# Kernel tuning notes

Hardware: AMD Instinct MI355X
Metric: run time of the kernel (lower is better)

## Reference

```python
import jax, jax.numpy as jnp
import numpy as np

D = 128
K = 8
TEMPERATURE = 1.0
LN_EPS = 1e-5
NORM_EPS = 1e-12


def setup_inputs() -> dict:
    key = jax.random.key(0)
    ks = jax.random.split(key, 6)
    B = 262144
    global_prosody = jax.random.normal(ks[0], (B, D), dtype=jnp.float32)
    W = jax.random.normal(ks[1], (D, D), dtype=jnp.float32) / np.sqrt(D)
    b = jnp.zeros((D,), dtype=jnp.float32)
    gamma = jnp.ones((D,), dtype=jnp.float32)
    beta = jnp.zeros((D,), dtype=jnp.float32)
    # codebook initialized as rows of an orthonormal basis (SVD of random init)
    init = jax.random.normal(ks[2], (D, K), dtype=jnp.float32)
    U, _, _ = jnp.linalg.svd(init, full_matrices=False)
    codebook = U[:, :K].T  # (K, D)
    return {"global_prosody": global_prosody, "W": W, "b": b,
            "gamma": gamma, "beta": beta, "codebook": codebook}


def _l2norm(x, axis=-1):
    n = jnp.sqrt(jnp.sum(x * x, axis=axis, keepdims=True))
    return x / jnp.maximum(n, NORM_EPS)


def reference(global_prosody, W, b, gamma, beta, codebook):
    # proj: Linear + LayerNorm
    h = global_prosody @ W.T + b                      # (B, D)
    mu = jnp.mean(h, axis=-1, keepdims=True)
    var = jnp.var(h, axis=-1, keepdims=True)
    h = (h - mu) / jnp.sqrt(var + LN_EPS) * gamma + beta
    # cosine-sim logits
    h_norm = _l2norm(h)                               # (B, D)
    cb_norm = _l2norm(codebook)                       # (K, D)
    logits = (h_norm @ cb_norm.T) / TEMPERATURE       # (B, K)
    soft_assign = jax.nn.softmax(logits, axis=-1)
    hard_indices = jnp.argmax(logits, axis=-1)        # (B,)
    hard_assign = jax.nn.one_hot(hard_indices, K, dtype=jnp.float32)
    # straight-through assignment
    assign = hard_assign + soft_assign - jax.lax.stop_gradient(soft_assign)
    embedding = assign @ codebook                     # (B, D)
    return hard_indices, soft_assign, embedding, logits
```

## Files before the change

### kernel.cpp

```cpp
#include <hip/hip_runtime.h>
#include <math.h>

#define DD 128
#define KK 8
#define LN_EPS 1e-5f
#define NORM_EPS 1e-12f

typedef __attribute__((ext_vector_type(8))) short bf16x8;
typedef __attribute__((ext_vector_type(4))) float f32x4;
typedef unsigned int uint;
typedef unsigned short ushort;

#define WSA_USHORTS (3 * 9 * 4 * 64 * 8)
#define G2B_OFF_F   (110592 / 4)
#define SCAL_OFF_F  (111616 / 4)

__device__ inline void split3(float x, uint& h, uint& m, uint& l) {
    uint u0 = __float_as_uint(x);
    uint rh = (u0 + 0x7FFFu + ((u0 >> 16) & 1u)) & 0xFFFF0000u;
    float xh = __uint_as_float(rh);
    float r1 = x - xh;
    uint u1 = __float_as_uint(r1);
    uint rm = (u1 + 0x7FFFu + ((u1 >> 16) & 1u)) & 0xFFFF0000u;
    float xm = __uint_as_float(rm);
    float r2 = r1 - xm;
    uint u2 = __float_as_uint(r2);
    uint rl = (u2 + 0x7FFFu + ((u2 >> 16) & 1u));
    h = rh; m = rm; l = rl;
}

__device__ inline void split2pack(float e0, float e1, uint& ph, uint& pm, uint& pl) {
    uint h0, m0, l0, h1, m1, l1;
    split3(e0, h0, m0, l0);
    split3(e1, h1, m1, l1);
    ph = (h0 >> 16) | (h1 & 0xFFFF0000u);
    pm = (m0 >> 16) | (m1 & 0xFFFF0000u);
    pl = (l0 >> 16) | (l1 & 0xFFFF0000u);
}

union FragU { uint4 u; bf16x8 f; };
union AccU  { f32x4 v; float a[4]; };

__global__ void l1q_prep0(const float* __restrict__ b, const float* __restrict__ gamma,
                          const float* __restrict__ beta, const float* __restrict__ cb,
                          float* __restrict__ ws)
{
    __shared__ float invn_s[KK];
    const int t = threadIdx.x;
    if (t < KK) {
        float s = 0.f;
        for (int j = 0; j < DD; ++j) { float v = cb[t * DD + j]; s = fmaf(v, v, s); }
        invn_s[t] = 1.0f / fmaxf(sqrtf(s), NORM_EPS);
    }
    __syncthreads();
    {
        float g = gamma[t];
        float* g2b = ws + G2B_OFF_F;
        g2b[2 * t]     = g * g;
        g2b[2 * t + 1] = b[t];
    }
    float* scal = ws + SCAL_OFF_F;
    if (t < KK) {
        float in = invn_s[t];
        float p = 0.f, q = 0.f, cu = 0.f;
        for (int j = 0; j < DD; ++j) {
            float c = cb[t * DD + j] * in;
            p  = fmaf(c, gamma[j], p);
            q  = fmaf(c, beta[j], q);
            cu = fmaf(c * gamma[j], b[j], cu);
        }
        scal[t]      = p;
        scal[8 + t]  = q;
        scal[22 + t] = cu;
    }
    if (t == 16) { float s = 0.f; for (int j = 0; j < DD; ++j) { float g = gamma[j]; s = fmaf(g, g, s); } scal[16] = s; }
    if (t == 17) { float s = 0.f; for (int j = 0; j < DD; ++j) s = fmaf(gamma[j], beta[j], s); scal[17] = s; }
    if (t == 18) { float s = 0.f; for (int j = 0; j < DD; ++j) { float v = beta[j]; s = fmaf(v, v, s); } scal[18] = s; }
    if (t == 19) { float s = 0.f; for (int j = 0; j < DD; ++j) s += b[j]; scal[19] = s; }
    if (t == 20) { float s = 0.f; for (int j = 0; j < DD; ++j) s = fmaf(gamma[j] * gamma[j], b[j], s); scal[20] = s; }
    if (t == 21) { float s = 0.f; for (int j = 0; j < DD; ++j) s = fmaf(gamma[j] * beta[j], b[j], s); scal[21] = s; }
}

__global__ void l1q_prepA(const float* __restrict__ W, const float* __restrict__ b,
                          const float* __restrict__ gamma, const float* __restrict__ beta,
                          const float* __restrict__ cb, ushort* __restrict__ wsA)
{
    __shared__ float invn_s[KK];
    __shared__ float we[11][DD];
    __shared__ float wext[16][32];
    const int t = threadIdx.x;
    const int jt = blockIdx.x >> 2;
    const int ks = blockIdx.x & 3;

    if (jt == 8) {
        if (t < KK) {
            float s = 0.f;
            for (int j = 0; j < DD; ++j) { float v = cb[t * DD + j]; s = fmaf(v, v, s); }
            invn_s[t] = 1.0f / fmaxf(sqrtf(s), NORM_EPS);
        }
        __syncthreads();
        for (int idx = t; idx < 11 * DD; idx += 256) {
            int e = idx / DD, j = idx % DD;
            float g = gamma[j];
            float v;
            if (e == 0)      v = 1.0f;
            else if (e == 1) v = g * g;
            else if (e == 2) v = g * beta[j];
            else             v = cb[(e - 3) * DD + j] * invn_s[e - 3] * g;
            we[e][j] = v;
        }
        __syncthreads();
    }

    for (int idx = t; idx < 512; idx += 256) {
        int jl = idx >> 5, kk = idx & 31;
        int k = ks * 32 + kk;
        float val;
        if (jt < 8) {
            val = W[(jt * 16 + jl) * DD + k];
        } else if (jl < 11) {
            float s = 0.f;
            for (int j = 0; j < DD; ++j) s = fmaf(we[jl][j], W[j * DD + k], s);
            val = s;
        } else {
            val = 0.f;
        }
        wext[jl][kk] = val;
    }
    __syncthreads();

    for (int idx = t; idx < 512; idx += 256) {
        int jl = idx >> 5, kk = idx & 31;
        int quad = kk >> 3, i = kk & 7;
        int lane = quad * 16 + jl;
        uint h, m, l;
        split3(wext[jl][kk], h, m, l);
        int base = jt * 4 + ks;
        wsA[(0 * 36 + base) * 512 + lane * 8 + i] = (ushort)(h >> 16);
        wsA[(1 * 36 + base) * 512 + lane * 8 + i] = (ushort)(m >> 16);
        wsA[(2 * 36 + base) * 512 + lane * 8 + i] = (ushort)(l >> 16);
    }
}

__global__ __launch_bounds__(256, 2)
void l1q_main(const float* __restrict__ x, const ushort* __restrict__ wsA,
              const float* __restrict__ wsf, const float* __restrict__ cb,
              float* __restrict__ out_idx, float* __restrict__ out_soft,
              float* __restrict__ out_emb, float* __restrict__ out_log,
              int B)
{
    __shared__ float g2b_s[256];
    __shared__ float scal_s[32];
    __shared__ float gath[4][320];
    __shared__ int   besti[4][64];

    const int t = threadIdx.x;
    const int wave = t >> 6;
    const int lane = t & 63;
    const int ml = lane & 15;
    const int q  = lane >> 4;
    const int rowbase = blockIdx.x * 256 + wave * 64;

    g2b_s[t] = wsf[G2B_OFF_F + t];
    if (t < 32) scal_s[t] = wsf[SCAL_OFF_F + t];
    __syncthreads();

    f32x4 acc[4][9];
    #pragma unroll
    for (int s = 0; s < 4; ++s)
        #pragma unroll
        for (int jt = 0; jt < 9; ++jt)
            acc[s][jt] = (f32x4){0.f, 0.f, 0.f, 0.f};

    for (int ks = 0; ks < 4; ++ks) {
        FragU xh[4], xm[4], xl[4];
        #pragma unroll
        for (int s = 0; s < 4; ++s) {
            const float* xp = x + (size_t)(rowbase + s * 16 + ml) * DD + ks * 32 + q * 8;
            float4 a = *(const float4*)xp;
            float4 c = *(const float4*)(xp + 4);
            split2pack(a.x, a.y, xh[s].u.x, xm[s].u.x, xl[s].u.x);
            split2pack(a.z, a.w, xh[s].u.y, xm[s].u.y, xl[s].u.y);
            split2pack(c.x, c.y, xh[s].u.z, xm[s].u.z, xl[s].u.z);
            split2pack(c.z, c.w, xh[s].u.w, xm[s].u.w, xl[s].u.w);
        }
        #pragma unroll
        for (int jt = 0; jt < 9; ++jt) {
            const int base = (jt * 4 + ks) * 512 + lane * 8;
            FragU wh, wm, wl;
            wh.u = *(const uint4*)(wsA + 0 * 36 * 512 + base);
            wm.u = *(const uint4*)(wsA + 1 * 36 * 512 + base);
            wl.u = *(const uint4*)(wsA + 2 * 36 * 512 + base);
            #pragma unroll
            for (int s = 0; s < 4; ++s) {
                f32x4 c = acc[s][jt];
                c = __builtin_amdgcn_mfma_f32_16x16x32_bf16(wl.f, xh[s].f, c, 0, 0, 0);
                c = __builtin_amdgcn_mfma_f32_16x16x32_bf16(wh.f, xl[s].f, c, 0, 0, 0);
                c = __builtin_amdgcn_mfma_f32_16x16x32_bf16(wm.f, xm[s].f, c, 0, 0, 0);
                c = __builtin_amdgcn_mfma_f32_16x16x32_bf16(wm.f, xh[s].f, c, 0, 0, 0);
                c = __builtin_amdgcn_mfma_f32_16x16x32_bf16(wh.f, xm[s].f, c, 0, 0, 0);
                c = __builtin_amdgcn_mfma_f32_16x16x32_bf16(wh.f, xh[s].f, c, 0, 0, 0);
                acc[s][jt] = c;
            }
        }
    }

    float s2a[4] = {0.f, 0.f, 0.f, 0.f};
    float t2a[4] = {0.f, 0.f, 0.f, 0.f};
    #pragma unroll
    for (int jt = 0; jt < 8; ++jt) {
        #pragma unroll
        for (int r = 0; r < 4; ++r) {
            int j = jt * 16 + q * 4 + r;
            float2 gb = *(const float2*)&g2b_s[2 * j];
            #pragma unroll
            for (int s = 0; s < 4; ++s) {
                AccU a; a.v = acc[s][jt];
                float h = a.a[r] + gb.y;
                float h2 = h * h;
                s2a[s] += h2;
                t2a[s] = fmaf(gb.x, h2, t2a[s]);
            }
        }
    }
    #pragma unroll
    for (int s = 0; s < 4; ++s) {
        s2a[s] += __shfl_xor(s2a[s], 16);
        s2a[s] += __shfl_xor(s2a[s], 32);
        t2a[s] += __shfl_xor(t2a[s], 16);
        t2a[s] += __shfl_xor(t2a[s], 32);
    }

    const float inv128 = 1.0f / 128.0f;
    const float cg2s = scal_s[16], cgbs = scal_s[17], cb2s = scal_s[18];
    const float cs1 = scal_s[19], ct1 = scal_s[20], cr1 = scal_s[21];

    #pragma unroll
    for (int s = 0; s < 4; ++s) {
        AccU mine; mine.v = acc[s][8];
        *(float4*)&gath[wave][ml * 20 + q * 4] = *(float4*)mine.a;
        __builtin_amdgcn_s_waitcnt(0);
        float4 A = *(const float4*)&gath[wave][ml * 20 + 0];
        float4 Bv = *(const float4*)&gath[wave][ml * 20 + 4];
        float4 C = *(const float4*)&gath[wave][ml * 20 + 8];

        float s1  = A.x + cs1;
        float t1  = A.y + ct1;
        float r1v = A.z + cr1;
        float u[KK] = {A.w + scal_s[22], Bv.x + scal_s[23], Bv.y + scal_s[24],
                       Bv.z + scal_s[25], Bv.w + scal_s[26], C.x + scal_s[27],
                       C.y + scal_s[28], C.z + scal_s[29]};

        float mu = s1 * inv128;
        float var = fmaf(-mu, mu, s2a[s] * inv128);
        float istd = 1.0f / sqrtf(var + LN_EPS);
        float nrm2 = istd * istd * (t2a[s] - 2.f * mu * t1 + mu * mu * cg2s)
                   + 2.f * istd * (r1v - mu * cgbs) + cb2s;
        float rinv = 1.0f / fmaxf(sqrtf(fmaxf(nrm2, 0.f)), NORM_EPS);

        float lg[KK];
        #pragma unroll
        for (int k = 0; k < KK; ++k)
            lg[k] = (istd * (u[k] - mu * scal_s[k]) + scal_s[8 + k]) * rinv;

        float mx = lg[0]; int bi = 0;
        #pragma unroll
        for (int k = 1; k < KK; ++k) if (lg[k] > mx) { mx = lg[k]; bi = k; }

        float ex[KK], se = 0.f;
        #pragma unroll
        for (int k = 0; k < KK; ++k) { ex[k] = expf(lg[k] - mx); se += ex[k]; }
        float rse = 1.0f / se;

        const int m = rowbase + s * 16 + ml;
        if (q == 0) {
            out_idx[m] = (float)bi;
            *(float4*)&out_log[(size_t)m * KK + 4] = make_float4(lg[4], lg[5], lg[6], lg[7]);
            besti[wave][s * 16 + ml] = bi;
        } else if (q == 1) {
            *(float4*)&out_soft[(size_t)m * KK] = make_float4(ex[0] * rse, ex[1] * rse, ex[2] * rse, ex[3] * rse);
        } else if (q == 2) {
            *(float4*)&out_soft[(size_t)m * KK + 4] = make_float4(ex[4] * rse, ex[5] * rse, ex[6] * rse, ex[7] * rse);
        } else {
            *(float4*)&out_log[(size_t)m * KK] = make_float4(lg[0], lg[1], lg[2], lg[3]);
        }
    }

    __builtin_amdgcn_s_waitcnt(0);
    const float4* cb4 = (const float4*)cb;
    float4* eo = (float4*)out_emb;
    #pragma unroll
    for (int s = 0; s < 4; ++s) {
        #pragma unroll
        for (int i = 0; i < 4; ++i) {
            int f4 = lane + 64 * i;
            int rl = f4 >> 5;
            int c  = f4 & 31;
            int k0 = besti[wave][s * 16 + rl];
            eo[(size_t)(rowbase + s * 16 + rl) * 32 + c] = cb4[k0 * 32 + c];
            int rl2 = (f4 + 256) >> 5;
            int k1 = besti[wave][s * 16 + rl2];
            eo[(size_t)(rowbase + s * 16 + rl2) * 32 + c] = cb4[k1 * 32 + c];
        }
    }
}

extern "C" void kernel_launch(void* const* d_in, const int* in_sizes, int n_in,
                              void* d_out, int out_size, void* d_ws, size_t ws_size,
                              hipStream_t stream) {
    const float* x     = (const float*)d_in[0];
    const float* W     = (const float*)d_in[1];
    const float* b     = (const float*)d_in[2];
    const float* gamma = (const float*)d_in[3];
    const float* beta  = (const float*)d_in[4];
    const float* cb    = (const float*)d_in[5];
    const int B = in_sizes[0] / DD;

    float*  ws  = (float*)d_ws;
    ushort* wsA = (ushort*)d_ws;

    float* out    = (float*)d_out;
    float* o_idx  = out;
    float* o_soft = out + (size_t)B;
    float* o_emb  = out + (size_t)B * (1 + KK);
    float* o_log  = out + (size_t)B * (1 + KK + DD);

    hipLaunchKernelGGL(l1q_prep0, dim3(1), dim3(128), 0, stream, b, gamma, beta, cb, ws);
    hipLaunchKernelGGL(l1q_prepA, dim3(36), dim3(256), 0, stream, W, b, gamma, beta, cb, wsA);
    const int grid = B / 256;
    hipLaunchKernelGGL(l1q_main, dim3(grid), dim3(256), 0, stream,
                       x, wsA, ws, cb, o_idx, o_soft, o_emb, o_log, B);
}
```

Before: 351.7 us.

## Stage split weights in LDS, use 16-row waves with 1024-thread blocks

The main kernel now runs 1024-thread blocks where each wave handles 16 rows instead of 64. The three-way bf16 split of W (about 108 KB) is copied into LDS once per block rather than read from global or L2 by every wave. The x row loads are software-prefetched one k-step ahead, and the x split switches to truncation plus v_perm packing instead of round-to-nearest bit arithmetic. This trades per-wave register reuse of W fragments across four row tiles for LDS reads and higher occupancy. It risks LDS capacity limits and a large staging cost per 256-row block.

```diff
diff --git a/kernel.cpp b/kernel.cpp
--- a/kernel.cpp
+++ b/kernel.cpp
@@ -11,7 +11,6 @@
 typedef unsigned int uint;
 typedef unsigned short ushort;
 
-#define WSA_USHORTS (3 * 9 * 4 * 64 * 8)
 #define G2B_OFF_F   (110592 / 4)
 #define SCAL_OFF_F  (111616 / 4)
 
@@ -29,13 +28,27 @@
     h = rh; m = rm; l = rl;
 }
 
-__device__ inline void split2pack(float e0, float e1, uint& ph, uint& pm, uint& pl) {
+__device__ inline void split3t(float x, uint& h, uint& m, uint& l) {
+    uint u0 = __float_as_uint(x);
+    float xh = __uint_as_float(u0 & 0xFFFF0000u);
+    float r1 = x - xh;
+    uint u1 = __float_as_uint(r1);
+    float xm = __uint_as_float(u1 & 0xFFFF0000u);
+    float r2 = r1 - xm;
+    h = u0; m = u1; l = __float_as_uint(r2);
+}
+
+__device__ inline uint packhi(uint a1, uint a0) {
+    return __builtin_amdgcn_perm(a1, a0, 0x07060302u);
+}
+
+__device__ inline void split2packt(float e0, float e1, uint& ph, uint& pm, uint& pl) {
     uint h0, m0, l0, h1, m1, l1;
-    split3(e0, h0, m0, l0);
-    split3(e1, h1, m1, l1);
-    ph = (h0 >> 16) | (h1 & 0xFFFF0000u);
-    pm = (m0 >> 16) | (m1 & 0xFFFF0000u);
-    pl = (l0 >> 16) | (l1 & 0xFFFF0000u);
+    split3t(e0, h0, m0, l0);
+    split3t(e1, h1, m1, l1);
+    ph = packhi(h1, h0);
+    pm = packhi(m1, m0);
+    pl = packhi(l1, l0);
 }
 
 union FragU { uint4 u; bf16x8 f; };
@@ -142,166 +155,158 @@
     }
 }
 
-__global__ __launch_bounds__(256, 2)
+__global__ __launch_bounds__(1024, 4)
 void l1q_main(const float* __restrict__ x, const ushort* __restrict__ wsA,
               const float* __restrict__ wsf, const float* __restrict__ cb,
               float* __restrict__ out_idx, float* __restrict__ out_soft,
               float* __restrict__ out_emb, float* __restrict__ out_log,
               int B)
 {
+    __shared__ uint4 Wl4[6912];
+    __shared__ float gath[16][320];
+    __shared__ int   besti[16][16];
     __shared__ float g2b_s[256];
     __shared__ float scal_s[32];
-    __shared__ float gath[4][320];
-    __shared__ int   besti[4][64];
 
     const int t = threadIdx.x;
     const int wave = t >> 6;
     const int lane = t & 63;
     const int ml = lane & 15;
     const int q  = lane >> 4;
-    const int rowbase = blockIdx.x * 256 + wave * 64;
-
-    g2b_s[t] = wsf[G2B_OFF_F + t];
-    if (t < 32) scal_s[t] = wsf[SCAL_OFF_F + t];
+    const int rowbase = blockIdx.x * 256 + wave * 16;
+    const int row = rowbase + ml;
+
+    const float* xp = x + (size_t)row * DD + q * 8;
+    float4 ra = *(const float4*)(xp + 0);
+    float4 rc = *(const float4*)(xp + 4);
+
+    {
+        const uint4* src = (const uint4*)wsA;
+        #pragma unroll
+        for (int i = 0; i < 7; ++i) {
+            int idx = t + i * 1024;
+            if (idx < 6912) Wl4[idx] = src[idx];
+        }
+    }
+    if (t < 256) g2b_s[t] = wsf[G2B_OFF_F + t];
+    if (t < 32)  scal_s[t] = wsf[SCAL_OFF_F + t];
     __syncthreads();
 
-    f32x4 acc[4][9];
-    #pragma unroll
-    for (int s = 0; s < 4; ++s)
-        #pragma unroll
-        for (int jt = 0; jt < 9; ++jt)
-            acc[s][jt] = (f32x4){0.f, 0.f, 0.f, 0.f};
-
+    f32x4 acc[9];
+    #pragma unroll
+    for (int jt = 0; jt < 9; ++jt) acc[jt] = (f32x4){0.f, 0.f, 0.f, 0.f};
+
+    #pragma unroll
     for (int ks = 0; ks < 4; ++ks) {
-        FragU xh[4], xm[4], xl[4];
-        #pragma unroll
-        for (int s = 0; s < 4; ++s) {
-            const float* xp = x + (size_t)(rowbase + s * 16 + ml) * DD + ks * 32 + q * 8;
-            float4 a = *(const float4*)xp;
-            float4 c = *(const float4*)(xp + 4);
-            split2pack(a.x, a.y, xh[s].u.x, xm[s].u.x, xl[s].u.x);
-            split2pack(a.z, a.w, xh[s].u.y, xm[s].u.y, xl[s].u.y);
-            split2pack(c.x, c.y, xh[s].u.z, xm[s].u.z, xl[s].u.z);
-            split2pack(c.z, c.w, xh[s].u.w, xm[s].u.w, xl[s].u.w);
-        }
+        int kn = ks < 3 ? ks + 1 : 3;
+        float4 na = *(const float4*)(xp + kn * 32 + 0);
+        float4 nc = *(const float4*)(xp + kn * 32 + 4);
+
+        FragU xh, xm, xl;
+        split2packt(ra.x, ra.y, xh.u.x, xm.u.x, xl.u.x);
+        split2packt(ra.z, ra.w, xh.u.y, xm.u.y, xl.u.y);
+        split2packt(rc.x, rc.y, xh.u.z, xm.u.z, xl.u.z);
+        split2packt(rc.z, rc.w, xh.u.w, xm.u.w, xl.u.w);
+
         #pragma unroll
         for (int jt = 0; jt < 9; ++jt) {
-            const int base = (jt * 4 + ks) * 512 + lane * 8;
+            const int pl = jt * 4 + ks;
             FragU wh, wm, wl;
-            wh.u = *(const uint4*)(wsA + 0 * 36 * 512 + base);
-            wm.u = *(const uint4*)(wsA + 1 * 36 * 512 + base);
-            wl.u = *(const uint4*)(wsA + 2 * 36 * 512 + base);
-            #pragma unroll
-            for (int s = 0; s < 4; ++s) {
-                f32x4 c = acc[s][jt];
-                c = __builtin_amdgcn_mfma_f32_16x16x32_bf16(wl.f, xh[s].f, c, 0, 0, 0);
-                c = __builtin_amdgcn_mfma_f32_16x16x32_bf16(wh.f, xl[s].f, c, 0, 0, 0);
-                c = __builtin_amdgcn_mfma_f32_16x16x32_bf16(wm.f, xm[s].f, c, 0, 0, 0);
-                c = __builtin_amdgcn_mfma_f32_16x16x32_bf16(wm.f, xh[s].f, c, 0, 0, 0);
-                c = __builtin_amdgcn_mfma_f32_16x16x32_bf16(wh.f, xm[s].f, c, 0, 0, 0);
-                c = __builtin_amdgcn_mfma_f32_16x16x32_bf16(wh.f, xh[s].f, c, 0, 0, 0);
-                acc[s][jt] = c;
-            }
-        }
-    }
-
-    float s2a[4] = {0.f, 0.f, 0.f, 0.f};
-    float t2a[4] = {0.f, 0.f, 0.f, 0.f};
+            wh.u = Wl4[(0 * 36 + pl) * 64 + lane];
+            wm.u = Wl4[(1 * 36 + pl) * 64 + lane];
+            wl.u = Wl4[(2 * 36 + pl) * 64 + lane];
+            f32x4 c = acc[jt];
+            c = __builtin_amdgcn_mfma_f32_16x16x32_bf16(wl.f, xh.f, c, 0, 0, 0);
+            c = __builtin_amdgcn_mfma_f32_16x16x32_bf16(wh.f, xl.f, c, 0, 0, 0);
+            c = __builtin_amdgcn_mfma_f32_16x16x32_bf16(wm.f, xm.f, c, 0, 0, 0);
+            c = __builtin_amdgcn_mfma_f32_16x16x32_bf16(wm.f, xh.f, c, 0, 0, 0);
+            c = __builtin_amdgcn_mfma_f32_16x16x32_bf16(wh.f, xm.f, c, 0, 0, 0);
+            c = __builtin_amdgcn_mfma_f32_16x16x32_bf16(wh.f, xh.f, c, 0, 0, 0);
+            acc[jt] = c;
+        }
+        ra = na; rc = nc;
+    }
+
+    float s2a = 0.f, t2a = 0.f;
     #pragma unroll
     for (int jt = 0; jt < 8; ++jt) {
+        AccU a; a.v = acc[jt];
         #pragma unroll
         for (int r = 0; r < 4; ++r) {
             int j = jt * 16 + q * 4 + r;
             float2 gb = *(const float2*)&g2b_s[2 * j];
-            #pragma unroll
-            for (int s = 0; s < 4; ++s) {
-                AccU a; a.v = acc[s][jt];
-                float h = a.a[r] + gb.y;
-                float h2 = h * h;
-                s2a[s] += h2;
-                t2a[s] = fmaf(gb.x, h2, t2a[s]);
-            }
-        }
-    }
-    #pragma unroll
-    for (int s = 0; s < 4; ++s) {
-        s2a[s] += __shfl_xor(s2a[s], 16);
-        s2a[s] += __shfl_xor(s2a[s], 32);
-        t2a[s] += __shfl_xor(t2a[s], 16);
-        t2a[s] += __shfl_xor(t2a[s], 32);
-    }
+            float h = a.a[r] + gb.y;
+            float h2 = h * h;
+            s2a += h2;
+            t2a = fmaf(gb.x, h2, t2a);
+        }
+    }
+    s2a += __shfl_xor(s2a, 16); s2a += __shfl_xor(s2a, 32);
+    t2a += __shfl_xor(t2a, 16); t2a += __shfl_xor(t2a, 32);
+
+    {
+        AccU mine; mine.v = acc[8];
+        *(float4*)&gath[wave][ml * 20 + q * 4] = *(float4*)mine.a;
+    }
+    __builtin_amdgcn_s_waitcnt(0);
+    float4 A  = *(const float4*)&gath[wave][ml * 20 + 0];
+    float4 Bv = *(const float4*)&gath[wave][ml * 20 + 4];
+    float4 C  = *(const float4*)&gath[wave][ml * 20 + 8];
 
     const float inv128 = 1.0f / 128.0f;
     const float cg2s = scal_s[16], cgbs = scal_s[17], cb2s = scal_s[18];
-    const float cs1 = scal_s[19], ct1 = scal_s[20], cr1 = scal_s[21];
-
-    #pragma unroll
-    for (int s = 0; s < 4; ++s) {
-        AccU mine; mine.v = acc[s][8];
-        *(float4*)&gath[wave][ml * 20 + q * 4] = *(float4*)mine.a;
-        __builtin_amdgcn_s_waitcnt(0);
-        float4 A = *(const float4*)&gath[wave][ml * 20 + 0];
-        float4 Bv = *(const float4*)&gath[wave][ml * 20 + 4];
-        float4 C = *(const float4*)&gath[wave][ml * 20 + 8];
-
-        float s1  = A.x + cs1;
-        float t1  = A.y + ct1;
-        float r1v = A.z + cr1;
-        float u[KK] = {A.w + scal_s[22], Bv.x + scal_s[23], Bv.y + scal_s[24],
-                       Bv.z + scal_s[25], Bv.w + scal_s[26], C.x + scal_s[27],
-                       C.y + scal_s[28], C.z + scal_s[29]};
-
-        float mu = s1 * inv128;
-        float var = fmaf(-mu, mu, s2a[s] * inv128);
-        float istd = 1.0f / sqrtf(var + LN_EPS);
-        float nrm2 = istd * istd * (t2a[s] - 2.f * mu * t1 + mu * mu * cg2s)
-                   + 2.f * istd * (r1v - mu * cgbs) + cb2s;
-        float rinv = 1.0f / fmaxf(sqrtf(fmaxf(nrm2, 0.f)), NORM_EPS);
-
-        float lg[KK];
-        #pragma unroll
-        for (int k = 0; k < KK; ++k)
-            lg[k] = (istd * (u[k] - mu * scal_s[k]) + scal_s[8 + k]) * rinv;
-
-        float mx = lg[0]; int bi = 0;
-        #pragma unroll
-        for (int k = 1; k < KK; ++k) if (lg[k] > mx) { mx = lg[k]; bi = k; }
-
-        float ex[KK], se = 0.f;
-        #pragma unroll
-        for (int k = 0; k < KK; ++k) { ex[k] = expf(lg[k] - mx); se += ex[k]; }
-        float rse = 1.0f / se;
-
-        const int m = rowbase + s * 16 + ml;
-        if (q == 0) {
-            out_idx[m] = (float)bi;
-            *(float4*)&out_log[(size_t)m * KK + 4] = make_float4(lg[4], lg[5], lg[6], lg[7]);
-            besti[wave][s * 16 + ml] = bi;
-        } else if (q == 1) {
-            *(float4*)&out_soft[(size_t)m * KK] = make_float4(ex[0] * rse, ex[1] * rse, ex[2] * rse, ex[3] * rse);
-        } else if (q == 2) {
-            *(float4*)&out_soft[(size_t)m * KK + 4] = make_float4(ex[4] * rse, ex[5] * rse, ex[6] * rse, ex[7] * rse);
-        } else {
-            *(float4*)&out_log[(size_t)m * KK] = make_float4(lg[0], lg[1], lg[2], lg[3]);
-        }
+
+    float s1  = A.x + scal_s[19];
+    float t1  = A.y + scal_s[20];
+    float r1v = A.z + scal_s[21];
+    float u[KK] = {A.w + scal_s[22], Bv.x + scal_s[23], Bv.y + scal_s[24],
+                   Bv.z + scal_s[25], Bv.w + scal_s[26], C.x + scal_s[27],
+                   C.y + scal_s[28], C.z + scal_s[29]};
+
+    float mu = s1 * inv128;
+    float var = fmaf(-mu, mu, s2a * inv128);
+    float istd = 1.0f / sqrtf(var + LN_EPS);
+    float nrm2 = istd * istd * (t2a - 2.f * mu * t1 + mu * mu * cg2s)
+               + 2.f * istd * (r1v - mu * cgbs) + cb2s;
+    float rinv = 1.0f / fmaxf(sqrtf(fmaxf(nrm2, 0.f)), NORM_EPS);
+
+    float lg[KK];
+    #pragma unroll
+    for (int k = 0; k < KK; ++k)
+        lg[k] = (istd * (u[k] - mu * scal_s[k]) + scal_s[8 + k]) * rinv;
+
+    float mx = lg[0]; int bi = 0;
+    #pragma unroll
+    for (int k = 1; k < KK; ++k) if (lg[k] > mx) { mx = lg[k]; bi = k; }
+
+    float ex[KK], se = 0.f;
+    #pragma unroll
+    for (int k = 0; k < KK; ++k) { ex[k] = expf(lg[k] - mx); se += ex[k]; }
+    float rse = 1.0f / se;
+
+    const int m = rowbase + ml;
+    if (q == 0) {
+        out_idx[m] = (float)bi;
+        *(float4*)&out_log[(size_t)m * KK + 4] = make_float4(lg[4], lg[5], lg[6], lg[7]);
+        besti[wave][ml] = bi;
+    } else if (q == 1) {
+        *(float4*)&out_soft[(size_t)m * KK] = make_float4(ex[0] * rse, ex[1] * rse, ex[2] * rse, ex[3] * rse);
+    } else if (q == 2) {
+        *(float4*)&out_soft[(size_t)m * KK + 4] = make_float4(ex[4] * rse, ex[5] * rse, ex[6] * rse, ex[7] * rse);
+    } else {
+        *(float4*)&out_log[(size_t)m * KK] = make_float4(lg[0], lg[1], lg[2], lg[3]);
     }
 
     __builtin_amdgcn_s_waitcnt(0);
     const float4* cb4 = (const float4*)cb;
     float4* eo = (float4*)out_emb;
     #pragma unroll
-    for (int s = 0; s < 4; ++s) {
-        #pragma unroll
-        for (int i = 0; i < 4; ++i) {
-            int f4 = lane + 64 * i;
-            int rl = f4 >> 5;
-            int c  = f4 & 31;
-            int k0 = besti[wave][s * 16 + rl];
-            eo[(size_t)(rowbase + s * 16 + rl) * 32 + c] = cb4[k0 * 32 + c];
-            int rl2 = (f4 + 256) >> 5;
-            int k1 = besti[wave][s * 16 + rl2];
-            eo[(size_t)(rowbase + s * 16 + rl2) * 32 + c] = cb4[k1 * 32 + c];
-        }
+    for (int i = 0; i < 8; ++i) {
+        int f4 = lane + 64 * i;
+        int rl = f4 >> 5;
+        int c  = f4 & 31;
+        int k0 = besti[wave][rl];
+        eo[(size_t)(rowbase + rl) * 32 + c] = cb4[k0 * 32 + c];
     }
 }
 
@@ -328,6 +333,6 @@
     hipLaunchKernelGGL(l1q_prep0, dim3(1), dim3(128), 0, stream, b, gamma, beta, cb, ws);
     hipLaunchKernelGGL(l1q_prepA, dim3(36), dim3(256), 0, stream, W, b, gamma, beta, cb, wsA);
     const int grid = B / 256;
-    hipLaunchKernelGGL(l1q_main, dim3(grid), dim3(256), 0, stream,
+    hipLaunchKernelGGL(l1q_main, dim3(grid), dim3(1024), 0, stream,
                        x, wsA, ws, cb, o_idx, o_soft, o_emb, o_log, B);
 }
```

Result: faster. 325.6 us (-7.4%).
